# Optimization experiments

Measured on AMD Instinct MI355X. Metric: run time of the kernel, lower is better.

## Reference

```python
import jax, jax.numpy as jnp
import numpy as np

EXP_SCALE = 10.0   # self.exp_param_scale
BETA_UP = 5.0      # self.kernel_beta_upbound
N_HEAD = 12


def setup_inputs() -> dict:
    key = jax.random.key(0)
    ks = jax.random.split(key, 7)
    B, T, C, nh = 2, 2048, 768, N_HEAD
    s = 1.0 / np.sqrt(C)
    x = jax.random.normal(ks[0], (B, T, C), jnp.float32)
    W_la = jax.random.normal(ks[1], (C, C), jnp.float32) * s      # LeakyAverage linear
    la_coef = jax.random.uniform(ks[2], (nh,), jnp.float32)        # per-head leaky decay in (0,1)
    W_v = jax.random.normal(ks[3], (C, C), jnp.float32) * s        # v_featurizer linear
    v_coef = jax.random.uniform(ks[4], (nh,), jnp.float32)         # v_featurizer per-head coef
    kernel_beta = jnp.ones((nh,), jnp.float32) / EXP_SCALE
    value_beta = jnp.ones((nh,), jnp.float32) * (-0.5 / EXP_SCALE)
    W_proj = jax.random.normal(ks[5], (C, C), jnp.float32) * s     # c_proj
    return dict(x=x, W_la=W_la, la_coef=la_coef, W_v=W_v, v_coef=v_coef,
                kernel_beta=kernel_beta, value_beta=value_beta, W_proj=W_proj)


def _leaky_average(x, W_la, la_coef):
    # y_t = c * y_{t-1} + (1-c) * (x W^T)_t, per-head decay c. Returns (B, nh, T, hs).
    B, T, C = x.shape
    nh = la_coef.shape[0]
    hs = C // nh
    u = (x @ W_la.T).reshape(B, T, nh, hs)
    c = la_coef[None, :, None]  # (1, nh, 1) broadcast over (B, nh, hs)

    def step(carry, ut):
        y = c * carry + (1.0 - c) * ut
        return y, y

    _, ys = jax.lax.scan(step, jnp.zeros((B, nh, hs), x.dtype), jnp.swapaxes(u, 0, 1))
    return jnp.transpose(ys, (1, 2, 0, 3))  # (T,B,nh,hs) -> (B,nh,T,hs)


def reference(x, W_la, la_coef, W_v, v_coef, kernel_beta, value_beta, W_proj):
    B, T, C = x.shape
    nh = la_coef.shape[0]
    hs = C // nh
    v_shift = 1

    # K path: leaky-average features, L2-normalize, exp-kernel beta scale
    k0 = _leaky_average(x, W_la, la_coef)                               # (B,nh,T,hs)
    raw_k = k0 / (jnp.linalg.norm(k0, axis=-1, keepdims=True) + 1e-6)
    beta = jnp.exp(jnp.minimum(kernel_beta * EXP_SCALE, BETA_UP))
    k = raw_k * beta[None, :, None, None]

    # V path: lowrlinearconv featurizer (linear, shift-by-1 mix, normalize) + value scale
    xl = (x @ W_v.T).reshape(B, T, nh, hs).transpose(0, 2, 1, 3)        # (B,nh,T,hs)
    shifted = jnp.concatenate([xl[:, :, 1:], jnp.zeros_like(xl[:, :, :1])], axis=2)
    vc = v_coef[None, :, None, None]
    vf = shifted * (1.0 - vc) + xl * vc
    vf = vf / (jnp.linalg.norm(vf, axis=-1, keepdims=True) + 1e-6)
    vbeta = jnp.exp(jnp.minimum(value_beta * EXP_SCALE, BETA_UP))
    v = vf * vbeta[None, :, None, None]

    # shifted-causal attention: query at position t (t>=1) attends keys 0..t-1, scale=1.0
    q = k[:, :, v_shift:]                                               # (B,nh,T-1,hs)
    scores = jnp.einsum('bhqd,bhkd->bhqk', q, k)                        # (B,nh,T-1,T)
    mask = jnp.tril(jnp.ones((T - v_shift, T), bool))                   # j <= iq  <=>  key < query pos
    scores = jnp.where(mask, scores, -jnp.inf)
    attn = jax.nn.softmax(scores, axis=-1)
    o = jnp.einsum('bhqk,bhkd->bhqd', attn, v)
    y = jnp.concatenate([jnp.zeros((B, nh, v_shift, hs), x.dtype), o], axis=2)

    y = y.transpose(0, 2, 1, 3).reshape(B, T, C)
    return y @ W_proj.T  # c_proj (dropouts are identity in eval)
```

## Files before the change

kernel.cpp:

```cpp
#include <hip/hip_runtime.h>
#include <hip/hip_bf16.h>
#include <math.h>

#define B_   2
#define T_   2048
#define C_   768
#define NH   12
#define HS   64
#define NSEG 64
#define SEGLEN 32
#define CX   1536

typedef __attribute__((ext_vector_type(8))) short short8;
typedef __attribute__((ext_vector_type(4))) short short4v;
typedef __attribute__((ext_vector_type(4))) float f32x4;

static __device__ inline unsigned short f2b(float f) {
  __hip_bfloat16 h = __float2bfloat16(f);
  unsigned short u;
  __builtin_memcpy(&u, &h, 2);
  return u;
}

#define GLOAD_LDS16(gp, lp)                                                        \
  __builtin_amdgcn_global_load_lds((const __attribute__((address_space(1))) void*)(gp), \
                                   (__attribute__((address_space(3))) void*)(lp), 16, 0, 0)

__global__ __launch_bounds__(256) void cast_all(const float* __restrict__ x,
                                                const float* __restrict__ wla,
                                                const float* __restrict__ wv,
                                                const float* __restrict__ wp,
                                                __hip_bfloat16* __restrict__ xb,
                                                __hip_bfloat16* __restrict__ wcat,
                                                __hip_bfloat16* __restrict__ wpb) {
  const int NX4 = (B_ * T_ * C_) / 4;
  const int NW4 = (C_ * C_) / 4;
  const int TOT = NX4 + 3 * NW4;
  int i = blockIdx.x * 256 + threadIdx.x;
  int st = gridDim.x * 256;
  for (; i < TOT; i += st) {
    const float* s;
    unsigned short* d;
    if (i < NX4) { s = x + (size_t)i * 4; d = (unsigned short*)xb + (size_t)i * 4; }
    else if (i < NX4 + NW4) { int j = i - NX4; s = wla + (size_t)j * 4; d = (unsigned short*)wcat + (size_t)j * 4; }
    else if (i < NX4 + 2 * NW4) { int j = i - NX4 - NW4; s = wv + (size_t)j * 4; d = (unsigned short*)wcat + (size_t)(C_ * C_) + (size_t)j * 4; }
    else { int j = i - NX4 - 2 * NW4; s = wp + (size_t)j * 4; d = (unsigned short*)wpb + (size_t)j * 4; }
    float4 v = *(const float4*)s;
    short4v o;
    o.x = (short)f2b(v.x); o.y = (short)f2b(v.y); o.z = (short)f2b(v.z); o.w = (short)f2b(v.w);
    *(short4v*)d = o;
  }
}

__global__ __launch_bounds__(256) void gemm_bf16(const __hip_bfloat16* __restrict__ A,
                                                 const __hip_bfloat16* __restrict__ Bw,
                                                 float* __restrict__ C,
                                                 int M, int N, int K) {
  __shared__ __hip_bfloat16 As[128 * 64];
  __shared__ __hip_bfloat16 Bs[128 * 64];
  const int tid = threadIdx.x;
  const int w = tid >> 6, lane = tid & 63;
  const int bm = blockIdx.x * 128, bn = blockIdx.y * 128;
  const int wr = w >> 1, wc = w & 1;

  f32x4 acc[4][4];
#pragma unroll
  for (int i = 0; i < 4; ++i)
#pragma unroll
    for (int j = 0; j < 4; ++j) acc[i][j] = (f32x4){0.f, 0.f, 0.f, 0.f};

  const int srow = (lane >> 3);
  const int soff0 = (lane & 7) * 16;
  const int sw = (lane & 7) << 4;

  for (int k0 = 0; k0 < K; k0 += 64) {
    __syncthreads();
#pragma unroll
    for (int c = 0; c < 8; ++c) {
      int gc = w * 8 + c;
      int isB = gc >> 4;
      int ci = gc & 15;
      int row = ci * 8 + srow;
      int soff = soff0 ^ ((row & 7) << 4);
      const __hip_bfloat16* gp =
          (isB ? Bw + (size_t)(bn + row) * K : A + (size_t)(bm + row) * K) + k0 + (soff >> 1);
      __hip_bfloat16* lp = (isB ? Bs : As) + ci * 512;
      GLOAD_LDS16(gp, lp);
    }
    __syncthreads();
#pragma unroll
    for (int ks = 0; ks < 2; ++ks) {
      short8 af[4], bf[4];
      const int colb = ks * 64 + (lane >> 4) * 16;
#pragma unroll
      for (int i = 0; i < 4; ++i) {
        int ra = wr * 64 + i * 16 + (lane & 15);
        int rb = wc * 64 + i * 16 + (lane & 15);
        af[i] = *(const short8*)((const char*)As + ra * 128 + (colb ^ sw));
        bf[i] = *(const short8*)((const char*)Bs + rb * 128 + (colb ^ sw));
      }
#pragma unroll
      for (int i = 0; i < 4; ++i)
#pragma unroll
        for (int j = 0; j < 4; ++j)
          acc[i][j] = __builtin_amdgcn_mfma_f32_16x16x32_bf16(af[i], bf[j], acc[i][j], 0, 0, 0);
    }
  }
#pragma unroll
  for (int i = 0; i < 4; ++i) {
#pragma unroll
    for (int r = 0; r < 4; ++r) {
      int m = bm + wr * 64 + i * 16 + (lane >> 4) * 4 + r;
      float* cp = C + (size_t)m * N + bn + wc * 64 + (lane & 15);
#pragma unroll
      for (int j = 0; j < 4; ++j) cp[j * 16] = acc[i][j][r];
    }
  }
}

__global__ __launch_bounds__(256) void scan_a(float* __restrict__ uxv,
                                              const float* __restrict__ la_coef,
                                              float* __restrict__ segend) {
  int cid = blockIdx.x * 4 + (threadIdx.x >> 6);
  int d   = threadIdx.x & 63;
  int seg = cid & (NSEG - 1);
  int bh  = cid >> 6;
  int h   = bh % NH;
  int b   = bh / NH;
  float c  = la_coef[h];
  float oc = 1.f - c;
  int t0 = seg * SEGLEN;
  float* up = uxv + ((size_t)b * T_ + t0) * CX + h * HS + d;
  float y = 0.f;
  for (int i = 0; i < SEGLEN; ++i) {
    float uv = up[(size_t)i * CX];
    y = fmaf(c, y, oc * uv);
    up[(size_t)i * CX] = y;
  }
  segend[(size_t)cid * HS + d] = y;
}

__global__ __launch_bounds__(256) void scan_b(const float* __restrict__ la_coef,
                                              const float* __restrict__ segend,
                                              float* __restrict__ carryin) {
  int s = blockIdx.x * 256 + threadIdx.x;
  if (s >= B_ * NH * HS) return;
  int d  = s & 63;
  int bh = s >> 6;
  int h  = bh % NH;
  float c = la_coef[h];
  float cl = c;
#pragma unroll
  for (int i = 0; i < 5; ++i) cl *= cl;
  float h0 = 0.f;
  for (int seg = 0; seg < NSEG; ++seg) {
    int cid = bh * NSEG + seg;
    carryin[(size_t)cid * HS + d] = h0;
    h0 = fmaf(cl, h0, segend[(size_t)cid * HS + d]);
  }
}

__global__ __launch_bounds__(256) void scan_c_norm(const float* __restrict__ la_coef,
                                                   const float* __restrict__ kernel_beta,
                                                   const float* __restrict__ carryin,
                                                   const float* __restrict__ uxv,
                                                   __hip_bfloat16* __restrict__ kb16) {
  int cid = blockIdx.x * 4 + (threadIdx.x >> 6);
  int d   = threadIdx.x & 63;
  int seg = cid & (NSEG - 1);
  int bh  = cid >> 6;
  int h   = bh % NH;
  int b   = bh / NH;
  float c  = la_coef[h];
  float bk = __expf(fminf(kernel_beta[h] * 10.f, 5.f));
  float hin = carryin[(size_t)cid * HS + d];
  int t0 = seg * SEGLEN;
  const float* kp = uxv + ((size_t)b * T_ + t0) * CX + h * HS + d;
  __hip_bfloat16* op = kb16 + ((size_t)bh * T_ + t0) * HS + d;
  float powc = c;
  for (int i = 0; i < SEGLEN; ++i) {
    float val = fmaf(powc, hin, kp[(size_t)i * CX]);
    powc *= c;
    float ss = val * val;
#pragma unroll
    for (int off = 1; off < 64; off <<= 1) ss += __shfl_xor(ss, off, 64);
    float scale = bk / (sqrtf(ss) + 1e-6f);
    op[(size_t)i * HS] = __float2bfloat16(val * scale);
  }
}

__global__ __launch_bounds__(256) void vbuild_t(const float* __restrict__ uxv,
                                                const float* __restrict__ v_coef,
                                                const float* __restrict__ value_beta,
                                                __hip_bfloat16* __restrict__ vt) {
  __shared__ __hip_bfloat16 sm[64][73];
  int t0 = blockIdx.x * 64;
  int bh = blockIdx.y;
  int h = bh % NH, b = bh / NH;
  int w = threadIdx.x >> 6, lane = threadIdx.x & 63;
  float vc = v_coef[h];
  float vb = __expf(fminf(value_beta[h] * 10.f, 5.f));
  for (int i = 0; i < 16; ++i) {
    int tl = w * 16 + i;
    int t = t0 + tl;
    const float* xp = uxv + ((size_t)b * T_ + t) * CX + 768 + h * HS + lane;
    float x0 = *xp;
    float x1 = (t + 1 < T_) ? xp[CX] : 0.f;
    float vf = (1.f - vc) * x1 + vc * x0;
    float ss = vf * vf;
#pragma unroll
    for (int off = 1; off < 64; off <<= 1) ss += __shfl_xor(ss, off, 64);
    sm[tl][lane] = __float2bfloat16(vf * vb / (sqrtf(ss) + 1e-6f));
  }
  __syncthreads();
  int d = threadIdx.x >> 3;
  int c = threadIdx.x & 7;
  for (int i = 0; i < 2; ++i) {
    int dd = d + i * 32;
    short8 v;
#pragma unroll
    for (int k = 0; k < 8; ++k)
      v[k] = (short)((const unsigned short*)&sm[c * 8 + k][dd])[0];
    *(short8*)((unsigned short*)vt + ((size_t)bh * HS + dd) * T_ + t0 + c * 8) = v;
  }
}

__global__ __launch_bounds__(256, 3) void attn5(const __hip_bfloat16* __restrict__ Kg,
                                                const __hip_bfloat16* __restrict__ Vtg,
                                                const float* __restrict__ kernel_beta,
                                                __hip_bfloat16* __restrict__ Y) {
  __shared__ __hip_bfloat16 Kt[2][64 * 64];
  __shared__ __hip_bfloat16 Vt[2][64 * 64];
  __shared__ char Pl[4][2304];
  const int bh = blockIdx.x;
  const int b = bh / NH, h = bh % NH;
  const int w = threadIdx.x >> 6, lane = threadIdx.x & 63;
  const int q16 = lane & 15, lg = lane >> 4;
  const int it = 31 - blockIdx.y;
  const int qb0 = 1 + it * 64;
  float bk = __expf(fminf(kernel_beta[h] * 10.f, 5.f));
  float m0 = bk * bk;
  const unsigned short* Kh = (const unsigned short*)Kg + (size_t)bh * T_ * HS;
  const unsigned short* Vh = (const unsigned short*)Vtg + (size_t)bh * HS * T_;
  unsigned short* Yh = (unsigned short*)Y + (size_t)b * T_ * C_ + h * HS;

  if (it == 0 && w == 0) Yh[lane] = 0;

  const int tq = qb0 + w * 16 + q16;
  short8 qf[2];
  {
    int tqc = tq > T_ - 1 ? T_ - 1 : tq;
#pragma unroll
    for (int ks = 0; ks < 2; ++ks)
      qf[ks] = *(const short8*)(Kh + (size_t)tqc * HS + ks * 32 + lg * 8);
  }

  f32x4 zero = {0.f, 0.f, 0.f, 0.f};
  f32x4 accO[4];
#pragma unroll
  for (int mt = 0; mt < 4; ++mt) accO[mt] = zero;
  float lsum = 0.f;

  char* pb = &Pl[w][0] + q16 * 144;
  const int swr = (q16 & 7) << 4;

  const int srow = lane >> 3;
  const int soff = ((lane & 7) << 4) ^ (srow << 4);

  const int NT = (qb0 + 126) >> 6;

#define STAGE_KV(buf, j0)                                                             \
  {                                                                                   \
    _Pragma("unroll")                                                                 \
    for (int n = 0; n < 2; ++n) {                                                     \
      int ch = w * 2 + n;                                                             \
      int row = ch * 8 + srow;                                                        \
      GLOAD_LDS16((const char*)(Kh + (size_t)((j0) + row) * HS) + soff,               \
                  &Kt[buf][ch * 512]);                                                \
      GLOAD_LDS16((const char*)(Vh + (size_t)row * T_ + (j0)) + soff,                 \
                  &Vt[buf][ch * 512]);                                                \
    }                                                                                 \
  }

  STAGE_KV(0, 0);
  asm volatile("s_waitcnt vmcnt(0)" ::: "memory");
  __syncthreads();

  for (int kt = 0; kt < NT; ++kt) {
    const int cur = kt & 1;
    const int j0 = kt * 64;
    if (kt + 1 < NT) STAGE_KV(cur ^ 1, j0 + 64);

    const char* Kb = (const char*)&Kt[cur][0];
    const char* Vb = (const char*)&Vt[cur][0];
    short8 kf[4][2], vf[4][2];
#pragma unroll
    for (int nt = 0; nt < 4; ++nt)
#pragma unroll
      for (int ks = 0; ks < 2; ++ks) {
        const int colb = ks * 64 + lg * 16;
        kf[nt][ks] = *(const short8*)(Kb + (nt * 16 + q16) * 128 + (colb ^ swr));
        vf[nt][ks] = *(const short8*)(Vb + (nt * 16 + q16) * 128 + (colb ^ swr));
      }
    f32x4 s[4];
#pragma unroll
    for (int nt = 0; nt < 4; ++nt) {
      s[nt] = __builtin_amdgcn_mfma_f32_16x16x32_bf16(kf[nt][0], qf[0], zero, 0, 0, 0);
      s[nt] = __builtin_amdgcn_mfma_f32_16x16x32_bf16(kf[nt][1], qf[1], s[nt], 0, 0, 0);
    }
#pragma unroll
    for (int nt = 0; nt < 4; ++nt) {
      float p[4];
#pragma unroll
      for (int r = 0; r < 4; ++r) {
        int j = j0 + nt * 16 + lg * 4 + r;
        p[r] = (j < tq) ? __expf(s[nt][r] - m0) : 0.f;
        lsum += p[r];
      }
      unsigned int w0, w1;
      asm("v_cvt_pk_bf16_f32 %0, %1, %2" : "=v"(w0) : "v"(p[0]), "v"(p[1]));
      asm("v_cvt_pk_bf16_f32 %0, %1, %2" : "=v"(w1) : "v"(p[2]), "v"(p[3]));
      uint2 pk; pk.x = w0; pk.y = w1;
      *(uint2*)(pb + nt * 32 + lg * 8) = pk;
    }
#pragma unroll
    for (int ks = 0; ks < 2; ++ks) {
      short8 pf = *(const short8*)(pb + ks * 64 + lg * 16);
#pragma unroll
      for (int mt = 0; mt < 4; ++mt)
        accO[mt] = __builtin_amdgcn_mfma_f32_16x16x32_bf16(vf[mt][ks], pf, accO[mt], 0, 0, 0);
    }
    asm volatile("s_waitcnt vmcnt(0)" ::: "memory");
    __syncthreads();
  }

  {
    float v = lsum;
    v += __shfl_xor(v, 16, 64);
    v += __shfl_xor(v, 32, 64);
    float inv = 1.f / v;
    if (tq < T_) {
      unsigned short* yp = Yh + (size_t)tq * C_;
#pragma unroll
      for (int mt = 0; mt < 4; ++mt) {
        float o0 = accO[mt][0] * inv, o1 = accO[mt][1] * inv;
        float o2 = accO[mt][2] * inv, o3 = accO[mt][3] * inv;
        unsigned int u0, u1;
        asm("v_cvt_pk_bf16_f32 %0, %1, %2" : "=v"(u0) : "v"(o0), "v"(o1));
        asm("v_cvt_pk_bf16_f32 %0, %1, %2" : "=v"(u1) : "v"(o2), "v"(o3));
        uint2 pk; pk.x = u0; pk.y = u1;
        *(uint2*)(yp + mt * 16 + lg * 4) = pk;
      }
    }
  }
#undef STAGE_KV
}

extern "C" void kernel_launch(void* const* d_in, const int* in_sizes, int n_in,
                              void* d_out, int out_size, void* d_ws, size_t ws_size,
                              hipStream_t stream) {
  const float* x          = (const float*)d_in[0];
  const float* W_la       = (const float*)d_in[1];
  const float* la_coef    = (const float*)d_in[2];
  const float* W_v        = (const float*)d_in[3];
  const float* v_coef     = (const float*)d_in[4];
  const float* kernel_bet = (const float*)d_in[5];
  const float* value_bet  = (const float*)d_in[6];
  const float* W_proj     = (const float*)d_in[7];
  float* out = (float*)d_out;

  float* ws = (float*)d_ws;
  const size_t NTOK = (size_t)B_ * T_ * C_;
  const size_t NSEGTOT = (size_t)B_ * NH * NSEG * HS;
  float* uxv     = ws;
  float* segend  = uxv + (size_t)B_ * T_ * CX;
  float* carryin = segend + NSEGTOT;
  __hip_bfloat16* kb16 = (__hip_bfloat16*)(carryin + NSEGTOT);
  __hip_bfloat16* vt16 = kb16 + NTOK;
  __hip_bfloat16* xb   = vt16 + NTOK;
  __hip_bfloat16* Wcat = xb + NTOK;
  __hip_bfloat16* Wpb  = Wcat + (size_t)CX * C_;
  __hip_bfloat16* yb   = xb;

  const int M = B_ * T_;

  cast_all<<<2048, 256, 0, stream>>>(x, W_la, W_v, W_proj, xb, Wcat, Wpb);

  gemm_bf16<<<dim3(M / 128, CX / 128), 256, 0, stream>>>(xb, Wcat, uxv, M, CX, C_);

  scan_a<<<dim3(B_ * NH * NSEG / 4), 256, 0, stream>>>(uxv, la_coef, segend);
  scan_b<<<dim3((B_ * NH * HS + 255) / 256), 256, 0, stream>>>(la_coef, segend, carryin);
  scan_c_norm<<<dim3(B_ * NH * NSEG / 4), 256, 0, stream>>>(la_coef, kernel_bet, carryin, uxv, kb16);

  vbuild_t<<<dim3(T_ / 64, B_ * NH), 256, 0, stream>>>(uxv, v_coef, value_bet, vt16);

  attn5<<<dim3(B_ * NH, 32), 256, 0, stream>>>(kb16, vt16, kernel_bet, yb);

  gemm_bf16<<<dim3(M / 128, C_ / 128), 256, 0, stream>>>(yb, Wpb, out, M, C_, C_);
}
```

Measured before the change: 114.1 us.

## Retune output GEMM tile, rework scan passes, and pipeline attention barriers

The GEMM is templated on its M tile so the output projection runs with 64-row tiles, giving more blocks on the small N=768 problem. The first scan pass no longer writes partial results back to the uxv buffer; the final pass recomputes the recurrence from the carried-in state, which saves one full write pass over the K features. The attention kernel now waits only on the previous stage's loads (vmcnt(4)) and uses raw barriers and setprio around its MFMA blocks, so loads overlap with compute. The partial vmcnt relies on the exact number of loads issued per stage.

```diff
diff --git a/kernel.cpp b/kernel.cpp
--- a/kernel.cpp
+++ b/kernel.cpp
@@ -52,34 +52,38 @@
   }
 }
 
+template <int BM>
 __global__ __launch_bounds__(256) void gemm_bf16(const __hip_bfloat16* __restrict__ A,
                                                  const __hip_bfloat16* __restrict__ Bw,
                                                  float* __restrict__ C,
                                                  int M, int N, int K) {
-  __shared__ __hip_bfloat16 As[128 * 64];
+  __shared__ __hip_bfloat16 As[BM * 64];
   __shared__ __hip_bfloat16 Bs[128 * 64];
   const int tid = threadIdx.x;
   const int w = tid >> 6, lane = tid & 63;
-  const int bm = blockIdx.x * 128, bn = blockIdx.y * 128;
-  const int wr = w >> 1, wc = w & 1;
-
-  f32x4 acc[4][4];
+  const int bm = blockIdx.x * BM, bn = blockIdx.y * 128;
+  const int q16 = lane & 15, lg = lane >> 4;
+
+  constexpr int NACC = (BM == 128) ? 4 : 2;
+  f32x4 acc[4][NACC];
 #pragma unroll
   for (int i = 0; i < 4; ++i)
 #pragma unroll
-    for (int j = 0; j < 4; ++j) acc[i][j] = (f32x4){0.f, 0.f, 0.f, 0.f};
+    for (int j = 0; j < NACC; ++j) acc[i][j] = (f32x4){0.f, 0.f, 0.f, 0.f};
 
   const int srow = (lane >> 3);
   const int soff0 = (lane & 7) * 16;
   const int sw = (lane & 7) << 4;
+  constexpr int ACH = BM / 8;
+  constexpr int CPW = (ACH + 16) / 4;
 
   for (int k0 = 0; k0 < K; k0 += 64) {
     __syncthreads();
 #pragma unroll
-    for (int c = 0; c < 8; ++c) {
-      int gc = w * 8 + c;
-      int isB = gc >> 4;
-      int ci = gc & 15;
+    for (int c = 0; c < CPW; ++c) {
+      int gc = w * CPW + c;
+      int isB = gc >= ACH;
+      int ci = isB ? gc - ACH : gc;
       int row = ci * 8 + srow;
       int soff = soff0 ^ ((row & 7) << 4);
       const __hip_bfloat16* gp =
@@ -90,19 +94,22 @@
     __syncthreads();
 #pragma unroll
     for (int ks = 0; ks < 2; ++ks) {
-      short8 af[4], bf[4];
-      const int colb = ks * 64 + (lane >> 4) * 16;
+      short8 af[4], bf[NACC];
+      const int colb = ks * 64 + lg * 16;
 #pragma unroll
       for (int i = 0; i < 4; ++i) {
-        int ra = wr * 64 + i * 16 + (lane & 15);
-        int rb = wc * 64 + i * 16 + (lane & 15);
+        int ra = (BM == 128) ? ((w >> 1) * 64 + i * 16 + q16) : (i * 16 + q16);
         af[i] = *(const short8*)((const char*)As + ra * 128 + (colb ^ sw));
-        bf[i] = *(const short8*)((const char*)Bs + rb * 128 + (colb ^ sw));
       }
 #pragma unroll
+      for (int j = 0; j < NACC; ++j) {
+        int rb = (BM == 128) ? ((w & 1) * 64 + j * 16 + q16) : (w * 32 + j * 16 + q16);
+        bf[j] = *(const short8*)((const char*)Bs + rb * 128 + (colb ^ sw));
+      }
+#pragma unroll
       for (int i = 0; i < 4; ++i)
 #pragma unroll
-        for (int j = 0; j < 4; ++j)
+        for (int j = 0; j < NACC; ++j)
           acc[i][j] = __builtin_amdgcn_mfma_f32_16x16x32_bf16(af[i], bf[j], acc[i][j], 0, 0, 0);
     }
   }
@@ -110,17 +117,19 @@
   for (int i = 0; i < 4; ++i) {
 #pragma unroll
     for (int r = 0; r < 4; ++r) {
-      int m = bm + wr * 64 + i * 16 + (lane >> 4) * 4 + r;
-      float* cp = C + (size_t)m * N + bn + wc * 64 + (lane & 15);
-#pragma unroll
-      for (int j = 0; j < 4; ++j) cp[j * 16] = acc[i][j][r];
-    }
-  }
-}
-
-__global__ __launch_bounds__(256) void scan_a(float* __restrict__ uxv,
-                                              const float* __restrict__ la_coef,
-                                              float* __restrict__ segend) {
+      int m = (BM == 128) ? (bm + (w >> 1) * 64 + i * 16 + lg * 4 + r)
+                          : (bm + i * 16 + lg * 4 + r);
+      int nb = (BM == 128) ? (bn + (w & 1) * 64 + q16) : (bn + w * 32 + q16);
+      float* cp = C + (size_t)m * N + nb;
+#pragma unroll
+      for (int j = 0; j < NACC; ++j) cp[j * 16] = acc[i][j][r];
+    }
+  }
+}
+
+__global__ __launch_bounds__(256) void scan_seg(const float* __restrict__ uxv,
+                                                const float* __restrict__ la_coef,
+                                                float* __restrict__ segend) {
   int cid = blockIdx.x * 4 + (threadIdx.x >> 6);
   int d   = threadIdx.x & 63;
   int seg = cid & (NSEG - 1);
@@ -130,13 +139,10 @@
   float c  = la_coef[h];
   float oc = 1.f - c;
   int t0 = seg * SEGLEN;
-  float* up = uxv + ((size_t)b * T_ + t0) * CX + h * HS + d;
+  const float* up = uxv + ((size_t)b * T_ + t0) * CX + h * HS + d;
   float y = 0.f;
-  for (int i = 0; i < SEGLEN; ++i) {
-    float uv = up[(size_t)i * CX];
-    y = fmaf(c, y, oc * uv);
-    up[(size_t)i * CX] = y;
-  }
+  for (int i = 0; i < SEGLEN; ++i)
+    y = fmaf(c, y, oc * up[(size_t)i * CX]);
   segend[(size_t)cid * HS + d] = y;
 }
 
@@ -172,20 +178,19 @@
   int h   = bh % NH;
   int b   = bh / NH;
   float c  = la_coef[h];
+  float oc = 1.f - c;
   float bk = __expf(fminf(kernel_beta[h] * 10.f, 5.f));
-  float hin = carryin[(size_t)cid * HS + d];
   int t0 = seg * SEGLEN;
-  const float* kp = uxv + ((size_t)b * T_ + t0) * CX + h * HS + d;
+  const float* up = uxv + ((size_t)b * T_ + t0) * CX + h * HS + d;
   __hip_bfloat16* op = kb16 + ((size_t)bh * T_ + t0) * HS + d;
-  float powc = c;
+  float y = carryin[(size_t)cid * HS + d];
   for (int i = 0; i < SEGLEN; ++i) {
-    float val = fmaf(powc, hin, kp[(size_t)i * CX]);
-    powc *= c;
-    float ss = val * val;
+    y = fmaf(c, y, oc * up[(size_t)i * CX]);
+    float ss = y * y;
 #pragma unroll
     for (int off = 1; off < 64; off <<= 1) ss += __shfl_xor(ss, off, 64);
     float scale = bk / (sqrtf(ss) + 1e-6f);
-    op[(size_t)i * HS] = __float2bfloat16(val * scale);
+    op[(size_t)i * HS] = __float2bfloat16(y * scale);
   }
 }
 
@@ -225,7 +230,7 @@
   }
 }
 
-__global__ __launch_bounds__(256, 3) void attn5(const __hip_bfloat16* __restrict__ Kg,
+__global__ __launch_bounds__(256, 3) void attn6(const __hip_bfloat16* __restrict__ Kg,
                                                 const __hip_bfloat16* __restrict__ Vtg,
                                                 const float* __restrict__ kernel_beta,
                                                 __hip_bfloat16* __restrict__ Y) {
@@ -283,13 +288,18 @@
   }
 
   STAGE_KV(0, 0);
-  asm volatile("s_waitcnt vmcnt(0)" ::: "memory");
-  __syncthreads();
 
   for (int kt = 0; kt < NT; ++kt) {
     const int cur = kt & 1;
     const int j0 = kt * 64;
-    if (kt + 1 < NT) STAGE_KV(cur ^ 1, j0 + 64);
+    if (kt + 1 < NT) {
+      STAGE_KV(cur ^ 1, j0 + 64);
+      asm volatile("s_waitcnt vmcnt(4)" ::: "memory");
+    } else {
+      asm volatile("s_waitcnt vmcnt(0)" ::: "memory");
+    }
+    __builtin_amdgcn_s_barrier();
+    __builtin_amdgcn_sched_barrier(0);
 
     const char* Kb = (const char*)&Kt[cur][0];
     const char* Vb = (const char*)&Vt[cur][0];
@@ -303,11 +313,13 @@
         vf[nt][ks] = *(const short8*)(Vb + (nt * 16 + q16) * 128 + (colb ^ swr));
       }
     f32x4 s[4];
+    __builtin_amdgcn_s_setprio(1);
 #pragma unroll
     for (int nt = 0; nt < 4; ++nt) {
       s[nt] = __builtin_amdgcn_mfma_f32_16x16x32_bf16(kf[nt][0], qf[0], zero, 0, 0, 0);
       s[nt] = __builtin_amdgcn_mfma_f32_16x16x32_bf16(kf[nt][1], qf[1], s[nt], 0, 0, 0);
     }
+    __builtin_amdgcn_s_setprio(0);
 #pragma unroll
     for (int nt = 0; nt < 4; ++nt) {
       float p[4];
@@ -323,6 +335,7 @@
       uint2 pk; pk.x = w0; pk.y = w1;
       *(uint2*)(pb + nt * 32 + lg * 8) = pk;
     }
+    __builtin_amdgcn_s_setprio(1);
 #pragma unroll
     for (int ks = 0; ks < 2; ++ks) {
       short8 pf = *(const short8*)(pb + ks * 64 + lg * 16);
@@ -330,8 +343,9 @@
       for (int mt = 0; mt < 4; ++mt)
         accO[mt] = __builtin_amdgcn_mfma_f32_16x16x32_bf16(vf[mt][ks], pf, accO[mt], 0, 0, 0);
     }
-    asm volatile("s_waitcnt vmcnt(0)" ::: "memory");
-    __syncthreads();
+    __builtin_amdgcn_s_setprio(0);
+    asm volatile("s_waitcnt lgkmcnt(0)" ::: "memory");
+    __builtin_amdgcn_s_barrier();
   }
 
   {
@@ -386,15 +400,15 @@
 
   cast_all<<<2048, 256, 0, stream>>>(x, W_la, W_v, W_proj, xb, Wcat, Wpb);
 
-  gemm_bf16<<<dim3(M / 128, CX / 128), 256, 0, stream>>>(xb, Wcat, uxv, M, CX, C_);
-
-  scan_a<<<dim3(B_ * NH * NSEG / 4), 256, 0, stream>>>(uxv, la_coef, segend);
+  gemm_bf16<128><<<dim3(M / 128, CX / 128), 256, 0, stream>>>(xb, Wcat, uxv, M, CX, C_);
+
+  scan_seg<<<dim3(B_ * NH * NSEG / 4), 256, 0, stream>>>(uxv, la_coef, segend);
   scan_b<<<dim3((B_ * NH * HS + 255) / 256), 256, 0, stream>>>(la_coef, segend, carryin);
   scan_c_norm<<<dim3(B_ * NH * NSEG / 4), 256, 0, stream>>>(la_coef, kernel_bet, carryin, uxv, kb16);
 
   vbuild_t<<<dim3(T_ / 64, B_ * NH), 256, 0, stream>>>(uxv, v_coef, value_bet, vt16);
 
-  attn5<<<dim3(B_ * NH, 32), 256, 0, stream>>>(kb16, vt16, kernel_bet, yb);
-
-  gemm_bf16<<<dim3(M / 128, C_ / 128), 256, 0, stream>>>(yb, Wpb, out, M, C_, C_);
-}
+  attn6<<<dim3(B_ * NH, 32), 256, 0, stream>>>(kb16, vt16, kernel_bet, yb);
+
+  gemm_bf16<64><<<dim3(M / 64, C_ / 128), 256, 0, stream>>>(yb, Wpb, out, M, C_, C_);
+}
```

After: 112.4 us. Within noise of the previous version (-1.5%).
